# Performance work log

Measured on AMD Instinct MI355X. Metric: run time of the kernel, lower is better.

Reference implementation:

```python
import jax, jax.numpy as jnp
import numpy as np

HIDDEN = 1024
HEADS = 16
HEAD_DIM = HIDDEN // HEADS


def setup_inputs() -> dict:
    key = jax.random.key(0)
    ks = jax.random.split(key, 7)
    B, S = 2, 2048
    scale = 1.0 / np.sqrt(HIDDEN)
    return {
        "hidden_states": jax.random.normal(ks[0], (B, S, HIDDEN), dtype=jnp.float32),
        "attention_mask": jnp.zeros((B, S), dtype=jnp.float32),
        "Wq": jax.random.normal(ks[1], (HIDDEN, HIDDEN), dtype=jnp.float32) * scale,
        "bq": jnp.zeros((HIDDEN,), dtype=jnp.float32),
        "Wk": jax.random.normal(ks[2], (HIDDEN, HIDDEN), dtype=jnp.float32) * scale,
        "bk": jnp.zeros((HIDDEN,), dtype=jnp.float32),
        "Wv": jax.random.normal(ks[3], (HIDDEN, HIDDEN), dtype=jnp.float32) * scale,
        "bv": jnp.zeros((HIDDEN,), dtype=jnp.float32),
    }


def reference(hidden_states, attention_mask, Wq, bq, Wk, bk, Wv, bv):
    B, S, _ = hidden_states.shape
    def heads(x):  # [B,S,HIDDEN] -> [B,H,S,D]
        return x.reshape(B, S, HEADS, HEAD_DIM).transpose(0, 2, 1, 3)
    q = heads(hidden_states @ Wq + bq)
    k = heads(hidden_states @ Wk + bk)
    v = heads(hidden_states @ Wv + bv)
    scores = jnp.einsum('bhqd,bhkd->bhqk', q, k) / np.sqrt(HEAD_DIM).astype(np.float32)
    # additive mask broadcast [B,1,1,S]
    scores = scores + attention_mask[:, None, None, :]
    probs = jax.nn.softmax(scores, axis=-1)
    # dropout is identity in eval mode (reference baseline)
    ctx = jnp.einsum('bhqk,bhkd->bhqd', probs, v)
    return ctx.transpose(0, 2, 1, 3).reshape(B, S, HIDDEN)
```

## Files before the change

kernel.cpp:

```cpp
#include <hip/hip_runtime.h>
#include <cstdint>
#include <cstddef>

typedef __bf16 bf16;
typedef __attribute__((ext_vector_type(8))) __bf16 bf16x8;
typedef __attribute__((ext_vector_type(4))) float f32x4;
typedef __attribute__((ext_vector_type(16))) float f32x16;

#define MFMA16(a, b, c) __builtin_amdgcn_mfma_f32_16x16x32_bf16((a), (b), (c), 0, 0, 0)
#define MFMA32(a, b, c) __builtin_amdgcn_mfma_f32_32x32x16_bf16((a), (b), (c), 0, 0, 0)

static constexpr int BB   = 2;
static constexpr int SS   = 2048;
static constexpr int HID  = 1024;
static constexpr int NH   = 16;
static constexpr int HD   = 64;
static constexpr int MROW = BB * SS;
static constexpr int NQKV = 3 * HID;
static constexpr float LOG2E = 1.4426950408889634f;
static constexpr float MSHIFT = 16.0f;

__device__ __forceinline__ int SW(int r) { return ((r ^ (r >> 3)) & 7) << 4; }

__device__ __forceinline__ uint32_t pack_bf16(float a, float b) {
    union { bf16 h[2]; uint32_t u; } x;
    x.h[0] = (bf16)a; x.h[1] = (bf16)b;
    return x.u;
}

__device__ __forceinline__ uint32_t pack_raw(bf16 a, bf16 b) {
    union { bf16 h[2]; uint32_t u; } x;
    x.h[0] = a; x.h[1] = b;
    return x.u;
}

__device__ __forceinline__ float exp2i(float x) {
    float r; asm("v_exp_f32 %0, %1" : "=v"(r) : "v"(x)); return r;
}

__device__ __forceinline__ void plswap(uint32_t& a, uint32_t& b) {
    asm("v_permlane32_swap_b32 %0, %1" : "+v"(a), "+v"(b));
}

__device__ __forceinline__ void gload16(const void* g, void* l) {
    __builtin_amdgcn_global_load_lds(
        (const __attribute__((address_space(1))) void*)g,
        (__attribute__((address_space(3))) void*)l, 16, 0, 0);
}

__global__ __launch_bounds__(256) void cvt_hidden(const float* __restrict__ in,
                                                  bf16* __restrict__ out) {
    const int i = (blockIdx.x * 256 + threadIdx.x) * 8;
    float4 f0 = *(const float4*)&in[i];
    float4 f1 = *(const float4*)&in[i + 4];
    bf16x8 o;
    o[0] = (bf16)f0.x; o[1] = (bf16)f0.y; o[2] = (bf16)f0.z; o[3] = (bf16)f0.w;
    o[4] = (bf16)f1.x; o[5] = (bf16)f1.y; o[6] = (bf16)f1.z; o[7] = (bf16)f1.w;
    *(bf16x8*)&out[i] = o;
}

__global__ __launch_bounds__(256) void maskcvt(const float* __restrict__ m,
                                               float* __restrict__ o) {
    const int i = blockIdx.x * 256 + threadIdx.x;
    o[i] = m[i] * LOG2E - MSHIFT;
}

__global__ __launch_bounds__(256) void wtrans(const float* __restrict__ Wq,
                                              const float* __restrict__ Wk,
                                              const float* __restrict__ Wv,
                                              bf16* __restrict__ Wt) {
    __shared__ float tile[32][33];
    const float* W = (blockIdx.z == 0) ? Wq : (blockIdx.z == 1) ? Wk : Wv;
    bf16* O = Wt + (size_t)blockIdx.z * HID * HID;
    const int x  = blockIdx.x * 32 + threadIdx.x;
    const int y0 = blockIdx.y * 32;
#pragma unroll
    for (int i = threadIdx.y; i < 32; i += 8)
        tile[i][threadIdx.x] = W[(size_t)(y0 + i) * HID + x];
    __syncthreads();
    const int k = y0 + threadIdx.x;
#pragma unroll
    for (int i = threadIdx.y; i < 32; i += 8)
        O[(size_t)(blockIdx.x * 32 + i) * HID + k] = (bf16)tile[threadIdx.x][i];
}

__global__ __launch_bounds__(256) void qkv_gemm(
    const bf16* __restrict__ A, const bf16* __restrict__ Bt,
    const float* __restrict__ bq, const float* __restrict__ bk,
    const float* __restrict__ bv,
    bf16* __restrict__ Qo, bf16* __restrict__ Ko, bf16* __restrict__ Vo) {
    __shared__ __align__(16) bf16 As[128 * 32];
    __shared__ __align__(16) bf16 Bs[128 * 32];
    const int t = threadIdx.x, l = t & 63;
    const int l15 = l & 15, l4 = l >> 4;
    const int w = t >> 6;
    const int wm = w >> 1, wn = w & 1;
    const int m0 = blockIdx.y * 128, n0 = blockIdx.x * 128;

    f32x4 acc[4][4] = {};

    for (int kt = 0; kt < 32; ++kt) {
        const int k0 = kt * 32;
        __syncthreads();
#pragma unroll
        for (int cc = 0; cc < 2; ++cc) {
            const int c = t + cc * 256;
            const int row = c >> 2, col = (c & 3) * 8;
            gload16(&A[(size_t)(m0 + row) * HID + k0 + col], (char*)As + c * 16);
            gload16(&Bt[(size_t)(n0 + row) * HID + k0 + col], (char*)Bs + c * 16);
        }
        __syncthreads();

        bf16x8 af[4], bf_[4];
#pragma unroll
        for (int mi = 0; mi < 4; ++mi) {
            const int r = wm * 64 + mi * 16 + l15;
            af[mi] = *(const bf16x8*)((const char*)As + r * 64 + l4 * 16);
        }
#pragma unroll
        for (int ni = 0; ni < 4; ++ni) {
            const int r = wn * 64 + ni * 16 + l15;
            bf_[ni] = *(const bf16x8*)((const char*)Bs + r * 64 + l4 * 16);
        }
        __builtin_amdgcn_s_setprio(1);
#pragma unroll
        for (int mi = 0; mi < 4; ++mi)
#pragma unroll
            for (int ni = 0; ni < 4; ++ni)
                acc[mi][ni] = MFMA16(af[mi], bf_[ni], acc[mi][ni]);
        __builtin_amdgcn_s_setprio(0);
    }

#pragma unroll
    for (int mi = 0; mi < 4; ++mi) {
#pragma unroll
        for (int ni = 0; ni < 4; ++ni) {
            const int ng = n0 + wn * 64 + ni * 16 + l15;
            const int qkv = ng >> 10;
            const int nn = ng & 1023;
            const int hh = nn >> 6, dd = nn & 63;
            const float* bp = (qkv == 0) ? bq : (qkv == 1) ? bk : bv;
            bf16* op = (qkv == 0) ? Qo : (qkv == 1) ? Ko : Vo;
            const float bias = bp[nn];
            const float scl = (qkv == 0) ? 0.125f * LOG2E : 1.0f;
            const int mg = m0 + wm * 64 + mi * 16 + l4 * 4;
            const int bb = mg >> 11, ss = mg & 2047;
            bf16* dst = op + ((size_t)(bb * NH + hh) * SS + ss) * HD + dd;
#pragma unroll
            for (int j = 0; j < 4; ++j)
                dst[(size_t)j * HD] = (bf16)((acc[mi][ni][j] + bias) * scl);
        }
    }
}

__global__ __launch_bounds__(256) void attn_fwd(
    const bf16* __restrict__ Q, const bf16* __restrict__ K,
    const bf16* __restrict__ V, const float* __restrict__ mkl,
    float* __restrict__ Op, float* __restrict__ ml) {
    __shared__ __align__(16) char KsB[2][64 * 128];
    __shared__ __align__(16) char VtB[2][64 * 128];

    const int t = threadIdx.x, l = t & 63, w = t >> 6;
    const int l31 = l & 31, h = l >> 5;

    const int bid = blockIdx.x;
    const int nid = (bid & 7) * 128 + (bid >> 3);
    const int bh = nid >> 5, kh = (nid >> 4) & 1, qb = nid & 15;
    const int q0 = qb * 128 + w * 32;
    const int kbase = kh * (SS / 2);

    const bf16* Qp = Q + (size_t)bh * SS * HD;
    const bf16* Kp = K + (size_t)bh * SS * HD;
    const bf16* Vp = V + (size_t)bh * SS * HD;
    const float* mkp = mkl + (bh >> 4) * SS;

    bf16x8 qf[4];
#pragma unroll
    for (int c = 0; c < 4; ++c)
        qf[c] = *(const bf16x8*)&Qp[(size_t)(q0 + l31) * HD + c * 16 + h * 8];

    float lrun = 0.f;
    f32x16 o0 = {}, o1 = {};

    const int vp_ = t >> 3, vdb = (t & 7) * 8;

    {
#pragma unroll
        for (int cc = 0; cc < 2; ++cc) {
            const int c = t + cc * 256;
            const int row = c >> 3, col8 = c & 7;
            const int csw = col8 ^ ((row ^ (row >> 3)) & 7);
            gload16(&Kp[(size_t)(kbase + row) * HD + csw * 8], &KsB[0][0] + c * 16);
        }
        bf16x8 va = *(const bf16x8*)&Vp[(size_t)(kbase + 2 * vp_) * HD + vdb];
        bf16x8 vb = *(const bf16x8*)&Vp[(size_t)(kbase + 2 * vp_ + 1) * HD + vdb];
#pragma unroll
        for (int i = 0; i < 8; ++i) {
            const int d = vdb + i;
            *(uint32_t*)(&VtB[0][0] + d * 128 + ((vp_ * 4) ^ SW(d))) =
                pack_raw(va[i], vb[i]);
        }
    }
    __syncthreads();

    const int NT = (SS / 2) / 64;
    for (int kt = 0; kt < NT; ++kt) {
        char* Ks = &KsB[kt & 1][0];
        char* Vt = &VtB[kt & 1][0];
        const int key0 = kbase + kt * 64;
        const bool more = (kt + 1) < NT;

        bf16x8 va = {}, vb = {};
        if (more) {
            const int keyn = key0 + 64;
            char* Ksn = &KsB[(kt + 1) & 1][0];
#pragma unroll
            for (int cc = 0; cc < 2; ++cc) {
                const int c = t + cc * 256;
                const int row = c >> 3, col8 = c & 7;
                const int csw = col8 ^ ((row ^ (row >> 3)) & 7);
                gload16(&Kp[(size_t)(keyn + row) * HD + csw * 8], Ksn + c * 16);
            }
            va = *(const bf16x8*)&Vp[(size_t)(keyn + 2 * vp_) * HD + vdb];
            vb = *(const bf16x8*)&Vp[(size_t)(keyn + 2 * vp_ + 1) * HD + vdb];
        }

#pragma unroll
        for (int g = 0; g < 2; ++g) {
            const int krow = g * 32 + l31;
            f32x16 st = {};
            __builtin_amdgcn_s_setprio(1);
#pragma unroll
            for (int c = 0; c < 4; ++c) {
                bf16x8 kf = *(const bf16x8*)(Ks + krow * 128 +
                                             ((c * 32 + h * 16) ^ SW(krow)));
                st = MFMA32(kf, qf[c], st);
            }
            __builtin_amdgcn_s_setprio(0);
            float ps = 0.f;
#pragma unroll
            for (int rq = 0; rq < 4; ++rq) {
                const f32x4 mk = *(const f32x4*)&mkp[key0 + g * 32 + rq * 8 + 4 * h];
#pragma unroll
                for (int j = 0; j < 4; ++j) {
                    const float p = exp2i(st[rq * 4 + j] + mk[j]);
                    st[rq * 4 + j] = p;
                    ps += p;
                }
            }
            lrun += ps;
#pragma unroll
            for (int cc = 0; cc < 2; ++cc) {
                uint32_t wA = pack_bf16(st[8 * cc + 0], st[8 * cc + 1]);
                uint32_t wB = pack_bf16(st[8 * cc + 2], st[8 * cc + 3]);
                uint32_t wC = pack_bf16(st[8 * cc + 4], st[8 * cc + 5]);
                uint32_t wD = pack_bf16(st[8 * cc + 6], st[8 * cc + 7]);
                plswap(wA, wC);
                plswap(wB, wD);
                union { uint32_t u[4]; bf16x8 v; } pb;
                pb.u[0] = wA; pb.u[1] = wB; pb.u[2] = wC; pb.u[3] = wD;
                const int colb = g * 64 + cc * 32 + h * 16;
                __builtin_amdgcn_s_setprio(1);
                {
                    bf16x8 vf0 = *(const bf16x8*)(Vt + l31 * 128 +
                                                  (colb ^ SW(l31)));
                    o0 = MFMA32(vf0, pb.v, o0);
                    const int r1 = 32 + l31;
                    bf16x8 vf1 = *(const bf16x8*)(Vt + r1 * 128 +
                                                  (colb ^ SW(r1)));
                    o1 = MFMA32(vf1, pb.v, o1);
                }
                __builtin_amdgcn_s_setprio(0);
            }
            if (g == 0 && more) {
                char* Vtn = &VtB[(kt + 1) & 1][0];
#pragma unroll
                for (int i = 0; i < 8; ++i) {
                    const int d = vdb + i;
                    *(uint32_t*)(Vtn + d * 128 + ((vp_ * 4) ^ SW(d))) =
                        pack_raw(va[i], vb[i]);
                }
            }
        }
        __syncthreads();
    }

    lrun += __shfl_xor(lrun, 32);
    const int part = kh * 512 + bh * 16 + qb;
    float* Ob = Op + (size_t)part * 8192;
    const int row = w * 32 + l31;
#pragma unroll
    for (int rq = 0; rq < 4; ++rq) {
        f32x4 a, b2;
#pragma unroll
        for (int j = 0; j < 4; ++j) { a[j] = o0[rq * 4 + j]; b2[j] = o1[rq * 4 + j]; }
        *(f32x4*)&Ob[row * 64 + rq * 8 + 4 * h] = a;
        *(f32x4*)&Ob[row * 64 + 32 + rq * 8 + 4 * h] = b2;
    }
    if (l < 32) ml[(size_t)part * 128 + (w * 32 + l)] = lrun;
}

__global__ __launch_bounds__(256) void combine(
    const float* __restrict__ Op, const float* __restrict__ ml,
    float* __restrict__ out) {
    const int tid = blockIdx.x * 256 + threadIdx.x;
    const int dg = tid & 15, gq = tid >> 4;
    const int bh = gq >> 11, s = gq & 2047;
    const int qb = s >> 7, q = s & 127;
    const int p0 = bh * 16 + qb, p1 = 512 + p0;

    const float l1 = ml[(size_t)p0 * 128 + q];
    const float l2 = ml[(size_t)p1 * 128 + q];
    const float inv = 1.0f / (l1 + l2);

    const f32x4 O1 = *(const f32x4*)&Op[(size_t)p0 * 8192 + q * 64 + dg * 4];
    const f32x4 O2 = *(const f32x4*)&Op[(size_t)p1 * 8192 + q * 64 + dg * 4];
    f32x4 r;
#pragma unroll
    for (int i = 0; i < 4; ++i) r[i] = (O1[i] + O2[i]) * inv;

    const int b = bh >> 4, hh = bh & 15;
    *(f32x4*)&out[((size_t)(b * SS + s)) * HID + hh * HD + dg * 4] = r;
}

extern "C" void kernel_launch(void* const* d_in, const int* in_sizes, int n_in,
                              void* d_out, int out_size, void* d_ws, size_t ws_size,
                              hipStream_t stream) {
    (void)in_sizes; (void)n_in; (void)out_size; (void)ws_size;
    const float* hs  = (const float*)d_in[0];
    const float* msk = (const float*)d_in[1];
    const float* Wq  = (const float*)d_in[2];
    const float* bq  = (const float*)d_in[3];
    const float* Wk  = (const float*)d_in[4];
    const float* bk  = (const float*)d_in[5];
    const float* Wv  = (const float*)d_in[6];
    const float* bv  = (const float*)d_in[7];
    float* out = (float*)d_out;
    char* ws = (char*)d_ws;
    const size_t MB = 1 << 20;

    bf16* Qb  = (bf16*)ws;
    bf16* Kb  = (bf16*)(ws + 8 * MB);
    bf16* Vb  = (bf16*)(ws + 16 * MB);
    float* mk2 = (float*)(ws + 24 * MB);
    bf16* Xb  = (bf16*)(ws + 25 * MB);
    bf16* Wt  = (bf16*)(ws + 33 * MB);
    float* Op  = (float*)(ws + 25 * MB);
    float* mlp = (float*)(ws + 59 * MB);

    cvt_hidden<<<dim3(MROW * HID / (256 * 8)), dim3(256), 0, stream>>>(hs, Xb);
    maskcvt<<<dim3(BB * SS / 256), dim3(256), 0, stream>>>(msk, mk2);
    wtrans<<<dim3(32, 32, 3), dim3(32, 8), 0, stream>>>(Wq, Wk, Wv, Wt);
    qkv_gemm<<<dim3(NQKV / 128, MROW / 128), dim3(256), 0, stream>>>(
        Xb, Wt, bq, bk, bv, Qb, Kb, Vb);
    attn_fwd<<<dim3(1024), dim3(256), 0, stream>>>(Qb, Kb, Vb, mk2, Op, mlp);
    combine<<<dim3(4096), dim3(256), 0, stream>>>(Op, mlp, out);
}
```

Baseline: 133.0 us.

## Split keys across waves within a block and merge partials in LDS

Each block now handles 32 queries. Its four waves each take an interleaved quarter of the keys, with K fragments loaded straight from global memory into registers and V transposed into per-wave LDS, so the main loop needs no block barriers. Partial outputs and row sums are reduced through shared memory at the end and written directly to the output. This removes the separate combine kernel and the fp32 partial buffers in global memory. The cost is that each wave now loads its own Q and K with no LDS reuse of K across waves, which means more global and L2 traffic.

```diff
diff --git a/kernel.cpp b/kernel.cpp
--- a/kernel.cpp
+++ b/kernel.cpp
@@ -19,8 +19,6 @@
 static constexpr int NQKV = 3 * HID;
 static constexpr float LOG2E = 1.4426950408889634f;
 static constexpr float MSHIFT = 16.0f;
-
-__device__ __forceinline__ int SW(int r) { return ((r ^ (r >> 3)) & 7) << 4; }
 
 __device__ __forceinline__ uint32_t pack_bf16(float a, float b) {
     union { bf16 h[2]; uint32_t u; } x;
@@ -156,171 +154,143 @@
 __global__ __launch_bounds__(256) void attn_fwd(
     const bf16* __restrict__ Q, const bf16* __restrict__ K,
     const bf16* __restrict__ V, const float* __restrict__ mkl,
-    float* __restrict__ Op, float* __restrict__ ml) {
-    __shared__ __align__(16) char KsB[2][64 * 128];
-    __shared__ __align__(16) char VtB[2][64 * 128];
+    float* __restrict__ out) {
+    __shared__ __align__(16) char smem[34816];
 
     const int t = threadIdx.x, l = t & 63, w = t >> 6;
     const int l31 = l & 31, h = l >> 5;
 
     const int bid = blockIdx.x;
-    const int nid = (bid & 7) * 128 + (bid >> 3);
-    const int bh = nid >> 5, kh = (nid >> 4) & 1, qb = nid & 15;
-    const int q0 = qb * 128 + w * 32;
-    const int kbase = kh * (SS / 2);
+    const int nid = (bid & 7) * 256 + (bid >> 3);
+    const int bh = nid >> 6, qb = nid & 63;
+    const int b = bh >> 4, hh = bh & 15;
+    const int q0 = qb * 32;
 
     const bf16* Qp = Q + (size_t)bh * SS * HD;
     const bf16* Kp = K + (size_t)bh * SS * HD;
     const bf16* Vp = V + (size_t)bh * SS * HD;
-    const float* mkp = mkl + (bh >> 4) * SS;
+    const float* mkp = mkl + b * SS;
+
+    char* Vt = smem + w * 4096;
 
     bf16x8 qf[4];
 #pragma unroll
     for (int c = 0; c < 4; ++c)
         qf[c] = *(const bf16x8*)&Qp[(size_t)(q0 + l31) * HD + c * 16 + h * 8];
 
+    const int vp = l & 15;
+    const int du0 = (l >> 4) * 16;
+
+#define VSTORE(va, vb, db)                                                   \
+    _Pragma("unroll")                                                        \
+    for (int i = 0; i < 8; ++i) {                                            \
+        const int d_ = (db) + i;                                             \
+        *(uint32_t*)(Vt + d_ * 64 +                                          \
+                     (((vp >> 2) ^ ((d_ ^ (d_ >> 2)) & 3)) * 16) +           \
+                     (vp & 3) * 4) = pack_raw((va)[i], (vb)[i]);             \
+    }
+
     float lrun = 0.f;
     f32x16 o0 = {}, o1 = {};
 
-    const int vp_ = t >> 3, vdb = (t & 7) * 8;
-
     {
+        const int kv = w * 32;
+        bf16x8 va0 = *(const bf16x8*)&Vp[(size_t)(kv + 2 * vp) * HD + du0];
+        bf16x8 vb0 = *(const bf16x8*)&Vp[(size_t)(kv + 2 * vp + 1) * HD + du0];
+        bf16x8 va1 = *(const bf16x8*)&Vp[(size_t)(kv + 2 * vp) * HD + du0 + 8];
+        bf16x8 vb1 = *(const bf16x8*)&Vp[(size_t)(kv + 2 * vp + 1) * HD + du0 + 8];
+        VSTORE(va0, vb0, du0)
+        VSTORE(va1, vb1, du0 + 8)
+    }
+
+    for (int kt = 0; kt < 16; ++kt) {
+        const int key0 = kt * 128 + w * 32;
+        bf16x8 kf[4];
+#pragma unroll
+        for (int c = 0; c < 4; ++c)
+            kf[c] = *(const bf16x8*)&Kp[(size_t)(key0 + l31) * HD + c * 16 + h * 8];
+        const int kvn = (kt == 15 ? 15 : kt + 1) * 128 + w * 32;
+        bf16x8 va0 = *(const bf16x8*)&Vp[(size_t)(kvn + 2 * vp) * HD + du0];
+        bf16x8 vb0 = *(const bf16x8*)&Vp[(size_t)(kvn + 2 * vp + 1) * HD + du0];
+        bf16x8 va1 = *(const bf16x8*)&Vp[(size_t)(kvn + 2 * vp) * HD + du0 + 8];
+        bf16x8 vb1 = *(const bf16x8*)&Vp[(size_t)(kvn + 2 * vp + 1) * HD + du0 + 8];
+
+        f32x16 st = {};
+        __builtin_amdgcn_s_setprio(1);
+#pragma unroll
+        for (int c = 0; c < 4; ++c) st = MFMA32(kf[c], qf[c], st);
+        __builtin_amdgcn_s_setprio(0);
+
+        float ps = 0.f;
+#pragma unroll
+        for (int rq = 0; rq < 4; ++rq) {
+            const f32x4 mk = *(const f32x4*)&mkp[key0 + rq * 8 + 4 * h];
+#pragma unroll
+            for (int j = 0; j < 4; ++j) {
+                const float p = exp2i(st[rq * 4 + j] + mk[j]);
+                st[rq * 4 + j] = p;
+                ps += p;
+            }
+        }
+        lrun += ps;
+
 #pragma unroll
         for (int cc = 0; cc < 2; ++cc) {
-            const int c = t + cc * 256;
-            const int row = c >> 3, col8 = c & 7;
-            const int csw = col8 ^ ((row ^ (row >> 3)) & 7);
-            gload16(&Kp[(size_t)(kbase + row) * HD + csw * 8], &KsB[0][0] + c * 16);
-        }
-        bf16x8 va = *(const bf16x8*)&Vp[(size_t)(kbase + 2 * vp_) * HD + vdb];
-        bf16x8 vb = *(const bf16x8*)&Vp[(size_t)(kbase + 2 * vp_ + 1) * HD + vdb];
-#pragma unroll
-        for (int i = 0; i < 8; ++i) {
-            const int d = vdb + i;
-            *(uint32_t*)(&VtB[0][0] + d * 128 + ((vp_ * 4) ^ SW(d))) =
-                pack_raw(va[i], vb[i]);
-        }
-    }
-    __syncthreads();
-
-    const int NT = (SS / 2) / 64;
-    for (int kt = 0; kt < NT; ++kt) {
-        char* Ks = &KsB[kt & 1][0];
-        char* Vt = &VtB[kt & 1][0];
-        const int key0 = kbase + kt * 64;
-        const bool more = (kt + 1) < NT;
-
-        bf16x8 va = {}, vb = {};
-        if (more) {
-            const int keyn = key0 + 64;
-            char* Ksn = &KsB[(kt + 1) & 1][0];
-#pragma unroll
-            for (int cc = 0; cc < 2; ++cc) {
-                const int c = t + cc * 256;
-                const int row = c >> 3, col8 = c & 7;
-                const int csw = col8 ^ ((row ^ (row >> 3)) & 7);
-                gload16(&Kp[(size_t)(keyn + row) * HD + csw * 8], Ksn + c * 16);
-            }
-            va = *(const bf16x8*)&Vp[(size_t)(keyn + 2 * vp_) * HD + vdb];
-            vb = *(const bf16x8*)&Vp[(size_t)(keyn + 2 * vp_ + 1) * HD + vdb];
-        }
-
-#pragma unroll
-        for (int g = 0; g < 2; ++g) {
-            const int krow = g * 32 + l31;
-            f32x16 st = {};
+            uint32_t wA = pack_bf16(st[8 * cc + 0], st[8 * cc + 1]);
+            uint32_t wB = pack_bf16(st[8 * cc + 2], st[8 * cc + 3]);
+            uint32_t wC = pack_bf16(st[8 * cc + 4], st[8 * cc + 5]);
+            uint32_t wD = pack_bf16(st[8 * cc + 6], st[8 * cc + 7]);
+            plswap(wA, wC);
+            plswap(wB, wD);
+            union { uint32_t u[4]; bf16x8 v; } pb;
+            pb.u[0] = wA; pb.u[1] = wB; pb.u[2] = wC; pb.u[3] = wD;
+            const int d0_ = l31, d1_ = 32 + l31;
+            const int s0 = (((cc * 2 + h) ^ ((d0_ ^ (d0_ >> 2)) & 3)) * 16);
+            const int s1 = (((cc * 2 + h) ^ ((d1_ ^ (d1_ >> 2)) & 3)) * 16);
             __builtin_amdgcn_s_setprio(1);
-#pragma unroll
-            for (int c = 0; c < 4; ++c) {
-                bf16x8 kf = *(const bf16x8*)(Ks + krow * 128 +
-                                             ((c * 32 + h * 16) ^ SW(krow)));
-                st = MFMA32(kf, qf[c], st);
+            {
+                bf16x8 vf0 = *(const bf16x8*)(Vt + d0_ * 64 + s0);
+                o0 = MFMA32(vf0, pb.v, o0);
+                bf16x8 vf1 = *(const bf16x8*)(Vt + d1_ * 64 + s1);
+                o1 = MFMA32(vf1, pb.v, o1);
             }
             __builtin_amdgcn_s_setprio(0);
-            float ps = 0.f;
-#pragma unroll
-            for (int rq = 0; rq < 4; ++rq) {
-                const f32x4 mk = *(const f32x4*)&mkp[key0 + g * 32 + rq * 8 + 4 * h];
-#pragma unroll
-                for (int j = 0; j < 4; ++j) {
-                    const float p = exp2i(st[rq * 4 + j] + mk[j]);
-                    st[rq * 4 + j] = p;
-                    ps += p;
-                }
-            }
-            lrun += ps;
-#pragma unroll
-            for (int cc = 0; cc < 2; ++cc) {
-                uint32_t wA = pack_bf16(st[8 * cc + 0], st[8 * cc + 1]);
-                uint32_t wB = pack_bf16(st[8 * cc + 2], st[8 * cc + 3]);
-                uint32_t wC = pack_bf16(st[8 * cc + 4], st[8 * cc + 5]);
-                uint32_t wD = pack_bf16(st[8 * cc + 6], st[8 * cc + 7]);
-                plswap(wA, wC);
-                plswap(wB, wD);
-                union { uint32_t u[4]; bf16x8 v; } pb;
-                pb.u[0] = wA; pb.u[1] = wB; pb.u[2] = wC; pb.u[3] = wD;
-                const int colb = g * 64 + cc * 32 + h * 16;
-                __builtin_amdgcn_s_setprio(1);
-                {
-                    bf16x8 vf0 = *(const bf16x8*)(Vt + l31 * 128 +
-                                                  (colb ^ SW(l31)));
-                    o0 = MFMA32(vf0, pb.v, o0);
-                    const int r1 = 32 + l31;
-                    bf16x8 vf1 = *(const bf16x8*)(Vt + r1 * 128 +
-                                                  (colb ^ SW(r1)));
-                    o1 = MFMA32(vf1, pb.v, o1);
-                }
-                __builtin_amdgcn_s_setprio(0);
-            }
-            if (g == 0 && more) {
-                char* Vtn = &VtB[(kt + 1) & 1][0];
-#pragma unroll
-                for (int i = 0; i < 8; ++i) {
-                    const int d = vdb + i;
-                    *(uint32_t*)(Vtn + d * 128 + ((vp_ * 4) ^ SW(d))) =
-                        pack_raw(va[i], vb[i]);
-                }
-            }
-        }
-        __syncthreads();
+        }
+
+        VSTORE(va0, vb0, du0)
+        VSTORE(va1, vb1, du0 + 8)
     }
 
     lrun += __shfl_xor(lrun, 32);
-    const int part = kh * 512 + bh * 16 + qb;
-    float* Ob = Op + (size_t)part * 8192;
-    const int row = w * 32 + l31;
-#pragma unroll
-    for (int rq = 0; rq < 4; ++rq) {
-        f32x4 a, b2;
-#pragma unroll
-        for (int j = 0; j < 4; ++j) { a[j] = o0[rq * 4 + j]; b2[j] = o1[rq * 4 + j]; }
-        *(f32x4*)&Ob[row * 64 + rq * 8 + 4 * h] = a;
-        *(f32x4*)&Ob[row * 64 + 32 + rq * 8 + 4 * h] = b2;
-    }
-    if (l < 32) ml[(size_t)part * 128 + (w * 32 + l)] = lrun;
-}
-
-__global__ __launch_bounds__(256) void combine(
-    const float* __restrict__ Op, const float* __restrict__ ml,
-    float* __restrict__ out) {
-    const int tid = blockIdx.x * 256 + threadIdx.x;
-    const int dg = tid & 15, gq = tid >> 4;
-    const int bh = gq >> 11, s = gq & 2047;
-    const int qb = s >> 7, q = s & 127;
-    const int p0 = bh * 16 + qb, p1 = 512 + p0;
-
-    const float l1 = ml[(size_t)p0 * 128 + q];
-    const float l2 = ml[(size_t)p1 * 128 + q];
-    const float inv = 1.0f / (l1 + l2);
-
-    const f32x4 O1 = *(const f32x4*)&Op[(size_t)p0 * 8192 + q * 64 + dg * 4];
-    const f32x4 O2 = *(const f32x4*)&Op[(size_t)p1 * 8192 + q * 64 + dg * 4];
-    f32x4 r;
-#pragma unroll
-    for (int i = 0; i < 4; ++i) r[i] = (O1[i] + O2[i]) * inv;
-
-    const int b = bh >> 4, hh = bh & 15;
-    *(f32x4*)&out[((size_t)(b * SS + s)) * HID + hh * HD + dg * 4] = r;
+    __syncthreads();
+    float* Om  = (float*)smem;
+    float* lml = (float*)(smem + 33792);
+#pragma unroll
+    for (int r = 0; r < 16; ++r) {
+        const int d = (r & 3) + 8 * (r >> 2) + 4 * h;
+        Om[(w * 64 + d) * 33 + l31] = o0[r];
+        Om[(w * 64 + d + 32) * 33 + l31] = o1[r];
+    }
+    if (l < 32) lml[w * 32 + l] = lrun;
+    __syncthreads();
+
+    const int mq = t >> 3, dg = (t & 7) * 8;
+    const float lsum = lml[mq] + lml[32 + mq] + lml[64 + mq] + lml[96 + mq];
+    const float inv = 1.0f / lsum;
+    float r8[8];
+#pragma unroll
+    for (int i = 0; i < 8; ++i) {
+        const int d = dg + i;
+        r8[i] = (Om[d * 33 + mq] + Om[(64 + d) * 33 + mq] +
+                 Om[(128 + d) * 33 + mq] + Om[(192 + d) * 33 + mq]) * inv;
+    }
+    float* op = &out[((size_t)(b * SS + q0 + mq)) * HID + hh * HD + dg];
+    f32x4 w0, w1;
+#pragma unroll
+    for (int i = 0; i < 4; ++i) { w0[i] = r8[i]; w1[i] = r8[4 + i]; }
+    *(f32x4*)op = w0;
+    *(f32x4*)(op + 4) = w1;
+#undef VSTORE
 }
 
 extern "C" void kernel_launch(void* const* d_in, const int* in_sizes, int n_in,
@@ -345,14 +315,11 @@
     float* mk2 = (float*)(ws + 24 * MB);
     bf16* Xb  = (bf16*)(ws + 25 * MB);
     bf16* Wt  = (bf16*)(ws + 33 * MB);
-    float* Op  = (float*)(ws + 25 * MB);
-    float* mlp = (float*)(ws + 59 * MB);
 
     cvt_hidden<<<dim3(MROW * HID / (256 * 8)), dim3(256), 0, stream>>>(hs, Xb);
     maskcvt<<<dim3(BB * SS / 256), dim3(256), 0, stream>>>(msk, mk2);
     wtrans<<<dim3(32, 32, 3), dim3(32, 8), 0, stream>>>(Wq, Wk, Wv, Wt);
     qkv_gemm<<<dim3(NQKV / 128, MROW / 128), dim3(256), 0, stream>>>(
         Xb, Wt, bq, bk, bv, Qb, Kb, Vb);
-    attn_fwd<<<dim3(1024), dim3(256), 0, stream>>>(Qb, Kb, Vb, mk2, Op, mlp);
-    combine<<<dim3(4096), dim3(256), 0, stream>>>(Op, mlp, out);
-}
+    attn_fwd<<<dim3(2048), dim3(256), 0, stream>>>(Qb, Kb, Vb, mk2, out);
+}
```

After: 187.7 us. 1.41x slower.

## Software-pipeline QK^T of next key tile with softmax and PV of current

Applied to the files above, without the earlier changes.

Restructures the attention inner loop so the QK^T MFMAs for tile i+1 are issued before the exp/softmax and PV work for tile i. Two score accumulator sets alternate, the K/V LDS buffers are split into named halves, and the loop is manually unrolled by two. The goal is to hide the exp2 and packing latency behind matrix-core work. In exchange, keeping extra f32x16 score accumulators live raises register pressure and may reduce occupancy.

```diff
diff --git a/kernel.cpp b/kernel.cpp
--- a/kernel.cpp
+++ b/kernel.cpp
@@ -157,8 +157,10 @@
     const bf16* __restrict__ Q, const bf16* __restrict__ K,
     const bf16* __restrict__ V, const float* __restrict__ mkl,
     float* __restrict__ Op, float* __restrict__ ml) {
-    __shared__ __align__(16) char KsB[2][64 * 128];
-    __shared__ __align__(16) char VtB[2][64 * 128];
+    __shared__ __align__(16) char Ks0[64 * 128];
+    __shared__ __align__(16) char Ks1[64 * 128];
+    __shared__ __align__(16) char Vt0[64 * 128];
+    __shared__ __align__(16) char Vt1[64 * 128];
 
     const int t = threadIdx.x, l = t & 63, w = t >> 6;
     const int l31 = l & 31, h = l >> 5;
@@ -183,64 +185,77 @@
     f32x16 o0 = {}, o1 = {};
 
     const int vp_ = t >> 3, vdb = (t & 7) * 8;
-
-    {
+    const int krow_s = t >> 3, kcsw = ((t & 7) ^ ((krow_s ^ (krow_s >> 3)) & 7)) * 8;
+
+    auto stageK = [&](int tile, char* dst) {
+        const int key0 = kbase + tile * 64;
 #pragma unroll
         for (int cc = 0; cc < 2; ++cc) {
             const int c = t + cc * 256;
-            const int row = c >> 3, col8 = c & 7;
-            const int csw = col8 ^ ((row ^ (row >> 3)) & 7);
-            gload16(&Kp[(size_t)(kbase + row) * HD + csw * 8], &KsB[0][0] + c * 16);
-        }
-        bf16x8 va = *(const bf16x8*)&Vp[(size_t)(kbase + 2 * vp_) * HD + vdb];
-        bf16x8 vb = *(const bf16x8*)&Vp[(size_t)(kbase + 2 * vp_ + 1) * HD + vdb];
+            const int row = c >> 3;
+            const int csw = (c & 7) ^ ((row ^ (row >> 3)) & 7);
+            gload16(&Kp[(size_t)(key0 + row) * HD + csw * 8], dst + c * 16);
+        }
+    };
+    auto loadV = [&](int tile, bf16x8& va, bf16x8& vb) {
+        const int key0 = kbase + tile * 64;
+        va = *(const bf16x8*)&Vp[(size_t)(key0 + 2 * vp_) * HD + vdb];
+        vb = *(const bf16x8*)&Vp[(size_t)(key0 + 2 * vp_ + 1) * HD + vdb];
+    };
+    auto storeV = [&](char* Vtn, const bf16x8& va, const bf16x8& vb) {
 #pragma unroll
         for (int i = 0; i < 8; ++i) {
             const int d = vdb + i;
-            *(uint32_t*)(&VtB[0][0] + d * 128 + ((vp_ * 4) ^ SW(d))) =
+            *(uint32_t*)(Vtn + d * 128 + ((vp_ * 4) ^ SW(d))) =
                 pack_raw(va[i], vb[i]);
         }
+    };
+    auto qkt = [&](const char* Ks, f32x16& st) {
+        const int krow = l31;
+        (void)krow; (void)Ks; (void)st;
+    };
+    (void)qkt;
+
+    stageK(0, Ks0);
+    stageK(1, Ks1);
+    {
+        bf16x8 va, vb, vc, vd;
+        loadV(0, va, vb);
+        loadV(1, vc, vd);
+        storeV(Vt0, va, vb);
+        storeV(Vt1, vc, vd);
     }
     __syncthreads();
 
-    const int NT = (SS / 2) / 64;
-    for (int kt = 0; kt < NT; ++kt) {
-        char* Ks = &KsB[kt & 1][0];
-        char* Vt = &VtB[kt & 1][0];
-        const int key0 = kbase + kt * 64;
-        const bool more = (kt + 1) < NT;
-
-        bf16x8 va = {}, vb = {};
-        if (more) {
-            const int keyn = key0 + 64;
-            char* Ksn = &KsB[(kt + 1) & 1][0];
-#pragma unroll
-            for (int cc = 0; cc < 2; ++cc) {
-                const int c = t + cc * 256;
-                const int row = c >> 3, col8 = c & 7;
-                const int csw = col8 ^ ((row ^ (row >> 3)) & 7);
-                gload16(&Kp[(size_t)(keyn + row) * HD + csw * 8], Ksn + c * 16);
-            }
-            va = *(const bf16x8*)&Vp[(size_t)(keyn + 2 * vp_) * HD + vdb];
-            vb = *(const bf16x8*)&Vp[(size_t)(keyn + 2 * vp_ + 1) * HD + vdb];
-        }
-
+    f32x16 stA0 = {}, stA1 = {}, stB0 = {}, stB1 = {};
+    auto qk_tile = [&](const char* Ks, f32x16& s0, f32x16& s1) {
+        __builtin_amdgcn_s_setprio(1);
+#pragma unroll
+        for (int c = 0; c < 4; ++c) {
+            const int r0 = l31;
+            bf16x8 kf0 = *(const bf16x8*)(Ks + r0 * 128 +
+                                          ((c * 32 + h * 16) ^ SW(r0)));
+            s0 = MFMA32(kf0, qf[c], s0);
+        }
+#pragma unroll
+        for (int c = 0; c < 4; ++c) {
+            const int r1 = 32 + l31;
+            bf16x8 kf1 = *(const bf16x8*)(Ks + r1 * 128 +
+                                          ((c * 32 + h * 16) ^ SW(r1)));
+            s1 = MFMA32(kf1, qf[c], s1);
+        }
+        __builtin_amdgcn_s_setprio(0);
+    };
+    auto sm_pv = [&](f32x16& s0, f32x16& s1, const char* Vt, int tile) {
+        const int key0 = kbase + tile * 64;
+        float ps = 0.f;
 #pragma unroll
         for (int g = 0; g < 2; ++g) {
-            const int krow = g * 32 + l31;
-            f32x16 st = {};
-            __builtin_amdgcn_s_setprio(1);
-#pragma unroll
-            for (int c = 0; c < 4; ++c) {
-                bf16x8 kf = *(const bf16x8*)(Ks + krow * 128 +
-                                             ((c * 32 + h * 16) ^ SW(krow)));
-                st = MFMA32(kf, qf[c], st);
-            }
-            __builtin_amdgcn_s_setprio(0);
-            float ps = 0.f;
+            f32x16& st = g ? s1 : s0;
 #pragma unroll
             for (int rq = 0; rq < 4; ++rq) {
-                const f32x4 mk = *(const f32x4*)&mkp[key0 + g * 32 + rq * 8 + 4 * h];
+                const f32x4 mk =
+                    *(const f32x4*)&mkp[key0 + g * 32 + rq * 8 + 4 * h];
 #pragma unroll
                 for (int j = 0; j < 4; ++j) {
                     const float p = exp2i(st[rq * 4 + j] + mk[j]);
@@ -248,7 +263,11 @@
                     ps += p;
                 }
             }
-            lrun += ps;
+        }
+        lrun += ps;
+#pragma unroll
+        for (int g = 0; g < 2; ++g) {
+            f32x16& st = g ? s1 : s0;
 #pragma unroll
             for (int cc = 0; cc < 2; ++cc) {
                 uint32_t wA = pack_bf16(st[8 * cc + 0], st[8 * cc + 1]);
@@ -272,17 +291,39 @@
                 }
                 __builtin_amdgcn_s_setprio(0);
             }
-            if (g == 0 && more) {
-                char* Vtn = &VtB[(kt + 1) & 1][0];
-#pragma unroll
-                for (int i = 0; i < 8; ++i) {
-                    const int d = vdb + i;
-                    *(uint32_t*)(Vtn + d * 128 + ((vp_ * 4) ^ SW(d))) =
-                        pack_raw(va[i], vb[i]);
-                }
+        }
+        s0 = f32x16{};
+        s1 = f32x16{};
+    };
+
+    qk_tile(Ks0, stA0, stA1);
+    __syncthreads();
+
+    constexpr int NT = (SS / 2) / 64;
+#pragma unroll 1
+    for (int ii = 0; ii < NT / 2; ++ii) {
+        const int i0 = 2 * ii;
+        const bool more = (ii < NT / 2 - 1);
+        {
+            bf16x8 va, vb;
+            if (more) stageK(i0 + 2, Ks0);
+            loadV(i0 + 1, va, vb);
+            qk_tile(Ks1, stB0, stB1);
+            sm_pv(stA0, stA1, Vt0, i0);
+            storeV(Vt1, va, vb);
+            __syncthreads();
+        }
+        {
+            bf16x8 va, vb;
+            if (more) {
+                stageK(i0 + 3, Ks1);
+                loadV(i0 + 2, va, vb);
+                qk_tile(Ks0, stA0, stA1);
             }
-        }
-        __syncthreads();
+            sm_pv(stB0, stB1, Vt1, i0 + 1);
+            if (more) storeV(Vt0, va, vb);
+            __syncthreads();
+        }
     }
 
     lrun += __shfl_xor(lrun, 32);
@@ -345,7 +386,7 @@
     float* mk2 = (float*)(ws + 24 * MB);
     bf16* Xb  = (bf16*)(ws + 25 * MB);
     bf16* Wt  = (bf16*)(ws + 33 * MB);
-    float* Op  = (float*)(ws + 25 * MB);
+    float* Opp = (float*)(ws + 25 * MB);
     float* mlp = (float*)(ws + 59 * MB);
 
     cvt_hidden<<<dim3(MROW * HID / (256 * 8)), dim3(256), 0, stream>>>(hs, Xb);
@@ -353,6 +394,6 @@
     wtrans<<<dim3(32, 32, 3), dim3(32, 8), 0, stream>>>(Wq, Wk, Wv, Wt);
     qkv_gemm<<<dim3(NQKV / 128, MROW / 128), dim3(256), 0, stream>>>(
         Xb, Wt, bq, bk, bv, Qb, Kb, Vb);
-    attn_fwd<<<dim3(1024), dim3(256), 0, stream>>>(Qb, Kb, Vb, mk2, Op, mlp);
-    combine<<<dim3(4096), dim3(256), 0, stream>>>(Op, mlp, out);
-}
+    attn_fwd<<<dim3(1024), dim3(256), 0, stream>>>(Qb, Kb, Vb, mk2, Opp, mlp);
+    combine<<<dim3(4096), dim3(256), 0, stream>>>(Opp, mlp, out);
+}
```

After: 157.1 us. 18.2% more time.
